# Optimization experiments

Measured on AMD Instinct MI355X. Metric: run time of the kernel, lower is better.

Reference implementation:

```python
import jax, jax.numpy as jnp
import numpy as np

N = 20000      # nodes
E = 320000     # edges
F = 128        # feat_dim
N_RBF = 20
CUTOFF = 5.0


def setup_inputs() -> dict:
    key = jax.random.key(0)
    ks = jax.random.split(key, 12)
    h_i = jax.random.normal(ks[0], (N, F), dtype=jnp.float32)
    v_i = jax.random.normal(ks[1], (N, F, 3), dtype=jnp.float32)
    # distances in (0, cutoff); keep strictly > 0 to avoid div-by-zero in sinc basis
    d_ij = (jax.random.uniform(ks[2], (E,), dtype=jnp.float32) * 0.98 + 0.01) * CUTOFF
    r = jax.random.normal(ks[3], (E, 3), dtype=jnp.float32)
    unit_r_ij = r / jnp.linalg.norm(r, axis=-1, keepdims=True)
    nbrs = jax.random.randint(ks[4], (E, 2), 0, N, dtype=jnp.int64)
    # params: layers = Dense(F->F, swish) then Dense(F->3F); dist_embed dense: n_rbf -> 3F
    s1 = 1.0 / np.sqrt(F)
    W1 = jax.random.uniform(ks[5], (F, F), jnp.float32, -s1, s1)
    b1 = jax.random.uniform(ks[6], (F,), jnp.float32, -s1, s1)
    W2 = jax.random.uniform(ks[7], (F, 3 * F), jnp.float32, -s1, s1)
    b2 = jax.random.uniform(ks[8], (3 * F,), jnp.float32, -s1, s1)
    sr = 1.0 / np.sqrt(N_RBF)
    Wr = jax.random.uniform(ks[9], (N_RBF, 3 * F), jnp.float32, -sr, sr)
    br = jax.random.uniform(ks[10], (3 * F,), jnp.float32, -sr, sr)
    return {"h_i": h_i, "v_i": v_i, "d_ij": d_ij, "unit_r_ij": unit_r_ij,
            "nbrs": nbrs, "W1": W1, "b1": b1, "W2": W2, "b2": b2, "Wr": Wr, "br": br}


def _dist_embed(d, Wr, br):
    # PaiNN sinc-like radial basis: sin(n*pi*d/cutoff)/d, n=1..N_RBF
    n = jnp.arange(1, N_RBF + 1, dtype=d.dtype)
    rbf = jnp.sin(n[None, :] * jnp.pi * d[:, None] / CUTOFF) / d[:, None]  # [E, N_RBF]
    # cosine cutoff envelope
    fcut = 0.5 * (jnp.cos(jnp.pi * d / CUTOFF) + 1.0) * (d < CUTOFF)       # [E]
    return (rbf @ Wr + br) * fcut[:, None]                                  # [E, 3F]


def reference(h_i, v_i, d_ij, unit_r_ij, nbrs, W1, b1, W2, b2, Wr, br):
    # phi = Dense(swish) -> Dense : [N, 3F]
    phi = jax.nn.silu(h_i @ W1 + b1) @ W2 + b2
    src = nbrs[:, 1]
    dst = nbrs[:, 0]
    edge_inv = phi[src] * _dist_embed(d_ij, Wr, br)          # [E, 3F]
    edge_inv = edge_inv.reshape(edge_inv.shape[0], 3, F)     # [E, 3, F]
    f1, f2, f3 = edge_inv[:, 0], edge_inv[:, 1], edge_inv[:, 2]
    # dv: [E, F, 3]
    dv = f1[:, :, None] * unit_r_ij[:, None, :] + f2[:, :, None] * v_i[src]
    dh_i = jax.ops.segment_sum(f3, dst, num_segments=N)      # [N, F]
    dv_i = jax.ops.segment_sum(dv, dst, num_segments=N)      # [N, F, 3]
    return (dh_i, dv_i)
```

## Files before the change

kernel.cpp:

```cpp
#include <hip/hip_runtime.h>
#include <math.h>

#define F 128
#define THREEF 384
#define N_RBF 20
#define CUTOFF 5.0f
#define CAP 64
#define TLDS_STRIDE 136

typedef __bf16 bf16x8 __attribute__((ext_vector_type(8)));
typedef float  f32x4  __attribute__((ext_vector_type(4)));

__global__ __launch_bounds__(256) void prep_kernel(
    const float* __restrict__ d_ij, const float* __restrict__ unit_r,
    const int* __restrict__ nbrs,
    const float* __restrict__ W1, const float* __restrict__ W2,
    const float* __restrict__ Wr,
    int* __restrict__ cnt, float* __restrict__ pack,
    __bf16* __restrict__ W1T, __bf16* __restrict__ W2T,
    float* __restrict__ WrT, int E, int EB)
{
    const int tid = threadIdx.x;
    const int b   = blockIdx.x;

    if (b < EB) {
        const int e = b * 256 + tid;
        if (e >= E) return;
        const int2 nb = ((const int2*)nbrs)[e];
        const int dst = nb.x;
        const int src = nb.y;
        const int slot = atomicAdd(&cnt[dst], 1);
        if (slot >= CAP) return;

        const float d = d_ij[e];
        const float x = (float)M_PI * d * (1.0f / CUTOFF);
        float sx, cx;
        __sincosf(x, &sx, &cx);
        const float fcut = (d < CUTOFF) ? 0.5f * (cx + 1.0f) : 0.0f;
        float4 q0, q1;
        q0.x = sx * fcut / d;
        q0.y = 2.0f * cx;
        q0.z = fcut;
        q0.w = unit_r[3 * e + 0];
        q1.x = unit_r[3 * e + 1];
        q1.y = unit_r[3 * e + 2];
        q1.z = __int_as_float(src);
        q1.w = 0.0f;
        float4* pk = (float4*)(pack + ((size_t)dst * CAP + slot) * 8);
        pk[0] = q0;
        pk[1] = q1;
    } else if (b < EB + 256) {
        const int idx = (b - EB) * 256 + tid;
        if (idx < 128 * 128) {
            const int n = idx >> 7, k = idx & 127;
            W1T[idx] = (__bf16)W1[k * F + n];
        }
        if (idx < 384 * 128) {
            const int n = idx >> 7, k = idx & 127;
            W2T[idx] = (__bf16)W2[k * THREEF + n];
        }
    } else {
        const int idx = (b - EB - 256) * 256 + tid;
        if (idx >= 5 * 3 * 128) return;
        const int f  = idx & 127;
        const int c  = (idx >> 7) % 3;
        const int n4 = idx / (3 * 128);
        float4 v;
        v.x = Wr[(4 * n4 + 0) * THREEF + c * 128 + f];
        v.y = Wr[(4 * n4 + 1) * THREEF + c * 128 + f];
        v.z = Wr[(4 * n4 + 2) * THREEF + c * 128 + f];
        v.w = Wr[(4 * n4 + 3) * THREEF + c * 128 + f];
        ((float4*)WrT)[idx] = v;
    }
}

__global__ __launch_bounds__(256) void mlp_mfma_kernel(
    const float* __restrict__ h,
    const __bf16* __restrict__ W1T,
    const float* __restrict__ b1,
    const __bf16* __restrict__ W2T,
    const float* __restrict__ b2,
    float* __restrict__ phi, int N)
{
    __shared__ __bf16 t_lds[4][16 * TLDS_STRIDE];

    const int wave = threadIdx.x >> 6;
    const int lane = threadIdx.x & 63;
    const int m    = lane & 15;
    const int quad = lane >> 4;
    const int node0 = blockIdx.x * 64 + wave * 16;
    if (node0 >= N) return;

    bf16x8 a1[4];
    #pragma unroll
    for (int kb = 0; kb < 4; ++kb) {
        const float* hp = h + (size_t)(node0 + m) * F + kb * 32 + quad * 8;
        const float4 x0 = *(const float4*)hp;
        const float4 x1 = *(const float4*)(hp + 4);
        bf16x8 a;
        a[0] = (__bf16)x0.x; a[1] = (__bf16)x0.y;
        a[2] = (__bf16)x0.z; a[3] = (__bf16)x0.w;
        a[4] = (__bf16)x1.x; a[5] = (__bf16)x1.y;
        a[6] = (__bf16)x1.z; a[7] = (__bf16)x1.w;
        a1[kb] = a;
    }

    #pragma unroll
    for (int ct = 0; ct < 8; ++ct) {
        f32x4 acc = {0.0f, 0.0f, 0.0f, 0.0f};
        #pragma unroll
        for (int kb = 0; kb < 4; ++kb) {
            const bf16x8 b =
                *(const bf16x8*)(W1T + (size_t)(ct * 16 + m) * F + kb * 32 + quad * 8);
            acc = __builtin_amdgcn_mfma_f32_16x16x32_bf16(a1[kb], b, acc, 0, 0, 0);
        }
        const int col = ct * 16 + m;
        const float bb = b1[col];
        #pragma unroll
        for (int reg = 0; reg < 4; ++reg) {
            const float x = acc[reg] + bb;
            const float s = x / (1.0f + __expf(-x));
            t_lds[wave][(quad * 4 + reg) * TLDS_STRIDE + col] = (__bf16)s;
        }
    }

    bf16x8 a2[4];
    #pragma unroll
    for (int kb = 0; kb < 4; ++kb)
        a2[kb] = *(const bf16x8*)&t_lds[wave][m * TLDS_STRIDE + kb * 32 + quad * 8];

    #pragma unroll
    for (int ct = 0; ct < 24; ++ct) {
        f32x4 acc = {0.0f, 0.0f, 0.0f, 0.0f};
        #pragma unroll
        for (int kb = 0; kb < 4; ++kb) {
            const bf16x8 b =
                *(const bf16x8*)(W2T + (size_t)(ct * 16 + m) * F + kb * 32 + quad * 8);
            acc = __builtin_amdgcn_mfma_f32_16x16x32_bf16(a2[kb], b, acc, 0, 0, 0);
        }
        const int col   = ct * 16 + m;
        const int plane = col >> 7;
        const int fc    = col & 127;
        const float bb  = b2[col];
        float* pp = phi + (size_t)plane * N * F + fc;
        #pragma unroll
        for (int reg = 0; reg < 4; ++reg) {
            const int row = quad * 4 + reg;
            pp[(size_t)(node0 + row) * F] = acc[reg] + bb;
        }
    }
}

__global__ __launch_bounds__(256, 4) void gather_kernel(
    const float* __restrict__ phi,
    const float* __restrict__ v_i,
    const float* __restrict__ WrT,
    const float* __restrict__ br,
    const int*   __restrict__ cnt,
    const float* __restrict__ pack,
    float* __restrict__ dh,
    float* __restrict__ dv,
    int N)
{
    __shared__ float4 s_pack[2][CAP * 2];

    const int tid  = threadIdx.x;
    const int half = tid >> 7;
    const int f    = tid & 127;
    const int node = blockIdx.x * 2 + half;

    const int deg0 = cnt[node];
    const int deg  = deg0 < CAP ? deg0 : CAP;

    {
        const float4* src = (const float4*)(pack + (size_t)node * CAP * 8);
        if (f < 2 * deg) s_pack[half][f] = src[f];
    }

    const float4* wTg = (const float4*)WrT;
    float4 w[15];
    #pragma unroll
    for (int j = 0; j < 15; ++j) w[j] = wTg[j * 128 + f];

    __syncthreads();

    const float br0 = br[f], br1 = br[f + 128], br2 = br[f + 256];

    const float* phi0 = phi;
    const float* phi1 = phi + (size_t)N * F;
    const float* phi2 = phi + (size_t)2 * N * F;

    float dh_acc = 0.0f, dv0 = 0.0f, dv1 = 0.0f, dv2 = 0.0f;

    for (int i = 0; i < deg; ++i) {
        const float* q = (const float*)&s_pack[half][2 * i];
        const float s1   = q[0];
        const float twoc = q[1];
        const float fcut = q[2];
        const float ux   = q[3];
        const float uy   = q[4];
        const float uz   = q[5];
        const int src = __builtin_amdgcn_readfirstlane(__float_as_int(q[6]));

        float a0 = br0 * fcut, a1 = br1 * fcut, a2 = br2 * fcut;
        float rp = 0.0f, rc = s1;
        #pragma unroll
        for (int n4 = 0; n4 < 5; ++n4) {
            const float4 w0 = w[n4 * 3 + 0];
            const float4 w1 = w[n4 * 3 + 1];
            const float4 w2 = w[n4 * 3 + 2];
            #pragma unroll
            for (int k = 0; k < 4; ++k) {
                const float wa = ((const float*)&w0)[k];
                const float wb = ((const float*)&w1)[k];
                const float wc = ((const float*)&w2)[k];
                a0 = fmaf(rc, wa, a0);
                a1 = fmaf(rc, wb, a1);
                a2 = fmaf(rc, wc, a2);
                const float rn = fmaf(twoc, rc, -rp);
                rp = rc;
                rc = rn;
            }
        }

        const float f1 = phi0[(size_t)src * F + f] * a0;
        const float f2 = phi1[(size_t)src * F + f] * a1;
        const float f3 = phi2[(size_t)src * F + f] * a2;

        dh_acc += f3;

        const float* vs = v_i + (size_t)src * THREEF + 3 * f;
        dv0 = fmaf(f1, ux, fmaf(f2, vs[0], dv0));
        dv1 = fmaf(f1, uy, fmaf(f2, vs[1], dv1));
        dv2 = fmaf(f1, uz, fmaf(f2, vs[2], dv2));
    }

    dh[(size_t)node * F + f] = dh_acc;
    float* dvp = dv + (size_t)node * THREEF + 3 * f;
    dvp[0] = dv0;
    dvp[1] = dv1;
    dvp[2] = dv2;
}

extern "C" void kernel_launch(void* const* d_in, const int* in_sizes, int n_in,
                              void* d_out, int out_size, void* d_ws, size_t ws_size,
                              hipStream_t stream) {
    const float* h_i    = (const float*)d_in[0];
    const float* v_i    = (const float*)d_in[1];
    const float* d_ij   = (const float*)d_in[2];
    const float* unit_r = (const float*)d_in[3];
    const int*   nbrs   = (const int*)  d_in[4];
    const float* W1     = (const float*)d_in[5];
    const float* b1     = (const float*)d_in[6];
    const float* W2     = (const float*)d_in[7];
    const float* b2     = (const float*)d_in[8];
    const float* Wr     = (const float*)d_in[9];
    const float* br     = (const float*)d_in[10];

    const int N = in_sizes[0] / F;
    const int E = in_sizes[2];

    float* dh = (float*)d_out;
    float* dv = dh + (size_t)N * F;

    float*  phi  = (float*)d_ws;
    float*  pack = phi + (size_t)3 * N * F;
    float*  WrT  = pack + (size_t)N * CAP * 8;
    int*    cnt  = (int*)(WrT + 5 * 3 * 128 * 4);
    __bf16* W1T  = (__bf16*)(cnt + N);
    __bf16* W2T  = W1T + 128 * 128;

    const int EB = (E + 255) / 256;

    hipMemsetAsync(cnt, 0, (size_t)N * sizeof(int), stream);

    prep_kernel<<<EB + 256 + 8, 256, 0, stream>>>(
        d_ij, unit_r, nbrs, W1, W2, Wr, cnt, pack, W1T, W2T, WrT, E, EB);
    mlp_mfma_kernel<<<(N + 63) / 64, 256, 0, stream>>>(h_i, W1T, b1, W2T, b2,
                                                       phi, N);
    gather_kernel<<<N / 2, 256, 0, stream>>>(phi, v_i, WrT, br, cnt, pack,
                                             dh, dv, N);
}
```

Baseline: 293.7 us.

## Interleave phi planes as float4 and precompute radial basis per edge in LDS

The MLP kernel now writes phi interleaved as [N, F, 4], so the gather kernel fetches all three per-feature values for a source node with one float4 load instead of three scattered loads from separate planes. The gather kernel also computes the Chebyshev-style sinc basis once per edge cooperatively into shared memory, so each thread no longer redundantly runs the recurrence. It keeps the Wr weights as 60 scalar registers pinned with empty asm. This costs 33% more phi memory (one padding lane), extra LDS and a second barrier, and adds register pressure against the occupancy-4 launch bound.

Result: slower. 318.6 us (+8.5%).

```diff
diff --git a/kernel.cpp b/kernel.cpp
--- a/kernel.cpp
+++ b/kernel.cpp
@@ -142,17 +142,16 @@
         const int plane = col >> 7;
         const int fc    = col & 127;
         const float bb  = b2[col];
-        float* pp = phi + (size_t)plane * N * F + fc;
         #pragma unroll
         for (int reg = 0; reg < 4; ++reg) {
             const int row = quad * 4 + reg;
-            pp[(size_t)(node0 + row) * F] = acc[reg] + bb;
+            phi[((((size_t)(node0 + row)) * F + fc) << 2) + plane] = acc[reg] + bb;
         }
     }
 }
 
 __global__ __launch_bounds__(256, 4) void gather_kernel(
-    const float* __restrict__ phi,
+    const float4* __restrict__ phi4,
     const float* __restrict__ v_i,
     const float* __restrict__ WrT,
     const float* __restrict__ br,
@@ -163,6 +162,7 @@
     int N)
 {
     __shared__ float4 s_pack[2][CAP * 2];
+    __shared__ float  s_rbf[2][CAP * 20];
 
     const int tid  = threadIdx.x;
     const int half = tid >> 7;
@@ -178,54 +178,63 @@
     }
 
     const float4* wTg = (const float4*)WrT;
-    float4 w[15];
-    #pragma unroll
-    for (int j = 0; j < 15; ++j) w[j] = wTg[j * 128 + f];
+    float w[60];
+    #pragma unroll
+    for (int j = 0; j < 15; ++j) {
+        const float4 t = wTg[j * 128 + f];
+        w[4 * j + 0] = t.x; w[4 * j + 1] = t.y;
+        w[4 * j + 2] = t.z; w[4 * j + 3] = t.w;
+    }
+    #pragma unroll
+    for (int j = 0; j < 60; ++j) asm volatile("" : "+v"(w[j]));
 
     __syncthreads();
 
+    if (f < deg) {
+        const float* q = (const float*)&s_pack[half][2 * f];
+        float rp = 0.0f, rc = q[0];
+        const float twoc = q[1];
+        float* rb = &s_rbf[half][f * 20];
+        rb[0] = rc;
+        #pragma unroll
+        for (int n = 1; n < 20; ++n) {
+            const float rn = fmaf(twoc, rc, -rp);
+            rp = rc; rc = rn;
+            rb[n] = rc;
+        }
+    }
+    __syncthreads();
+
     const float br0 = br[f], br1 = br[f + 128], br2 = br[f + 256];
-
-    const float* phi0 = phi;
-    const float* phi1 = phi + (size_t)N * F;
-    const float* phi2 = phi + (size_t)2 * N * F;
 
     float dh_acc = 0.0f, dv0 = 0.0f, dv1 = 0.0f, dv2 = 0.0f;
 
     for (int i = 0; i < deg; ++i) {
         const float* q = (const float*)&s_pack[half][2 * i];
-        const float s1   = q[0];
-        const float twoc = q[1];
         const float fcut = q[2];
         const float ux   = q[3];
         const float uy   = q[4];
         const float uz   = q[5];
         const int src = __builtin_amdgcn_readfirstlane(__float_as_int(q[6]));
 
+        const float* rb = &s_rbf[half][i * 20];
+
         float a0 = br0 * fcut, a1 = br1 * fcut, a2 = br2 * fcut;
-        float rp = 0.0f, rc = s1;
         #pragma unroll
         for (int n4 = 0; n4 < 5; ++n4) {
-            const float4 w0 = w[n4 * 3 + 0];
-            const float4 w1 = w[n4 * 3 + 1];
-            const float4 w2 = w[n4 * 3 + 2];
             #pragma unroll
             for (int k = 0; k < 4; ++k) {
-                const float wa = ((const float*)&w0)[k];
-                const float wb = ((const float*)&w1)[k];
-                const float wc = ((const float*)&w2)[k];
-                a0 = fmaf(rc, wa, a0);
-                a1 = fmaf(rc, wb, a1);
-                a2 = fmaf(rc, wc, a2);
-                const float rn = fmaf(twoc, rc, -rp);
-                rp = rc;
-                rc = rn;
+                const float rn = rb[n4 * 4 + k];
+                a0 = fmaf(rn, w[(n4 * 3 + 0) * 4 + k], a0);
+                a1 = fmaf(rn, w[(n4 * 3 + 1) * 4 + k], a1);
+                a2 = fmaf(rn, w[(n4 * 3 + 2) * 4 + k], a2);
             }
         }
 
-        const float f1 = phi0[(size_t)src * F + f] * a0;
-        const float f2 = phi1[(size_t)src * F + f] * a1;
-        const float f3 = phi2[(size_t)src * F + f] * a2;
+        const float4 ph = phi4[(size_t)src * F + f];
+        const float f1 = ph.x * a0;
+        const float f2 = ph.y * a1;
+        const float f3 = ph.z * a2;
 
         dh_acc += f3;
 
@@ -264,7 +273,7 @@
     float* dv = dh + (size_t)N * F;
 
     float*  phi  = (float*)d_ws;
-    float*  pack = phi + (size_t)3 * N * F;
+    float*  pack = phi + (size_t)4 * N * F;
     float*  WrT  = pack + (size_t)N * CAP * 8;
     int*    cnt  = (int*)(WrT + 5 * 3 * 128 * 4);
     __bf16* W1T  = (__bf16*)(cnt + N);
@@ -278,6 +287,6 @@
         d_ij, unit_r, nbrs, W1, W2, Wr, cnt, pack, W1T, W2T, WrT, E, EB);
     mlp_mfma_kernel<<<(N + 63) / 64, 256, 0, stream>>>(h_i, W1T, b1, W2T, b2,
                                                        phi, N);
-    gather_kernel<<<N / 2, 256, 0, stream>>>(phi, v_i, WrT, br, cnt, pack,
-                                             dh, dv, N);
-}
+    gather_kernel<<<N / 2, 256, 0, stream>>>((const float4*)phi, v_i, WrT, br,
+                                             cnt, pack, dh, dv, N);
+}
```
